# Performance work log

Measured on AMD Instinct MI355X. Metric: run time of the kernel, lower is better.

## Reference

```python
import jax, jax.numpy as jnp
import numpy as np

N_NODES = 100000
HIDDEN = 64
N_LAYERS = 4
N_EDGES = 800000
EPS = 1e-5  # equinox RMSNorm default


def rmsnorm(x, w):
    # per-node RMSNorm over last dim, learned scale, no bias
    inv = jax.lax.rsqrt(jnp.mean(x * x, axis=-1, keepdims=True) + EPS)
    return x * inv * w


def setup_inputs() -> dict:
    key = jax.random.key(0)
    ks = jax.random.split(key, 5)
    x = jax.random.normal(ks[0], (N_NODES, HIDDEN), dtype=jnp.float32)
    # eqx Linear weight (out,in), init ~ U(-1/sqrt(in), 1/sqrt(in)); randn*scale is fine for a baseline
    scale = 1.0 / np.sqrt(HIDDEN)
    conv_w = jax.random.normal(ks[1], (N_LAYERS, HIDDEN, HIDDEN), dtype=jnp.float32) * scale
    hid_w = jax.random.normal(ks[2], (N_LAYERS, HIDDEN, HIDDEN), dtype=jnp.float32) * scale
    conv_norm_w = jnp.ones((N_LAYERS, HIDDEN), dtype=jnp.float32)
    hid_norm_w = jnp.ones((N_LAYERS, HIDDEN), dtype=jnp.float32)
    row = jax.random.randint(ks[3], (N_EDGES,), 0, N_NODES, dtype=jnp.int32)
    col = jax.random.randint(ks[4], (N_EDGES,), 0, N_NODES, dtype=jnp.int32)
    return {"x": x, "conv_w": conv_w, "conv_norm_w": conv_norm_w,
            "hid_w": hid_w, "hid_norm_w": hid_norm_w, "row": row, "col": col}


def reference(x, conv_w, conv_norm_w, hid_w, hid_norm_w, row, col):
    n_nodes = x.shape[0]

    def step(h, params):
        cw, cnw, hw, hnw = params
        # GConvLayer: linear (no bias) -> relu -> sparse adjacency aggregation -> residual RMSNorm
        m = jax.nn.relu(h @ cw.T)                                  # [n_nodes, d]
        agg = jax.ops.segment_sum(m[col], row, num_segments=n_nodes)  # a @ m (unweighted COO)
        h = rmsnorm(h + agg, cnw)
        # HiddenLayer: linear -> relu -> residual RMSNorm
        y = jax.nn.relu(h @ hw.T)
        h = rmsnorm(h + y, hnw)
        return h, None

    x, _ = jax.lax.scan(step, x, (conv_w, conv_norm_w, hid_w, hid_norm_w))
    return x
```

## Files before the change

### kernel.cpp

```cpp
#include <hip/hip_runtime.h>
#include <hip/hip_bf16.h>

#define HIDDEN 64
#define EPS 1e-5f
#define NPB 64
#define NPB2 128
#define WST 72

typedef __attribute__((ext_vector_type(8))) short bf16x8;
typedef __attribute__((ext_vector_type(4))) float f32x4;

__device__ __forceinline__ unsigned short f2b(float x) {
    __hip_bfloat16 b = __float2bfloat16(x);
    return *(unsigned short*)&b;
}
__device__ __forceinline__ float b2f(unsigned short u) {
    unsigned int ui = (unsigned int)u << 16;
    return *(float*)&ui;
}
__device__ __forceinline__ float b2f_lo(unsigned int u) { unsigned int ui = u << 16; return *(float*)&ui; }
__device__ __forceinline__ float b2f_hi(unsigned int u) { unsigned int ui = u & 0xffff0000u; return *(float*)&ui; }


__global__ __launch_bounds__(256) void hist_rank_kernel(const int* __restrict__ row,
                                                        int* __restrict__ cnt,
                                                        int* __restrict__ erank, int e) {
    int stride = gridDim.x * blockDim.x;
    for (int i = blockIdx.x * blockDim.x + threadIdx.x; i < e; i += stride) {
        int r = row[i];
        erank[i] = atomicAdd(&cnt[r], 1);
    }
}

__global__ __launch_bounds__(256) void block_sum_kernel(const int* __restrict__ cnt,
                                                        int* __restrict__ bsum, int n) {
    __shared__ int wsum[4];
    int tid = threadIdx.x;
    int i = blockIdx.x * 256 + tid;
    int v = (i < n) ? cnt[i] : 0;
#pragma unroll
    for (int off = 32; off > 0; off >>= 1) v += __shfl_xor(v, off, 64);
    if ((tid & 63) == 0) wsum[tid >> 6] = v;
    __syncthreads();
    if (tid == 0) bsum[blockIdx.x] = wsum[0] + wsum[1] + wsum[2] + wsum[3];
}

__global__ __launch_bounds__(1024) void scan_bsum_kernel(int* __restrict__ bsum, int nb,
                                                         int* __restrict__ total_out) {
    __shared__ int wsum[16];
    __shared__ int wexcl[16];
    int tid = threadIdx.x;
    int lane = tid & 63;
    int w = tid >> 6;
    int v = (tid < nb) ? bsum[tid] : 0;
    int sc = v;
#pragma unroll
    for (int off = 1; off < 64; off <<= 1) {
        int t = __shfl_up(sc, off, 64);
        if (lane >= off) sc += t;
    }
    if (lane == 63) wsum[w] = sc;
    __syncthreads();
    if (tid == 0) {
        int a = 0;
#pragma unroll
        for (int j = 0; j < 16; j++) { wexcl[j] = a; a += wsum[j]; }
        *total_out = a;
    }
    __syncthreads();
    if (tid < nb) bsum[tid] = wexcl[w] + (sc - v);
}

__global__ __launch_bounds__(256) void scan_final_kernel(const int* __restrict__ cnt,
                                                         const int* __restrict__ bexcl,
                                                         int* __restrict__ row_ptr, int n) {
    __shared__ int wsum[4];
    __shared__ int wexcl[4];
    int tid = threadIdx.x;
    int lane = tid & 63;
    int w = tid >> 6;
    int i = blockIdx.x * 256 + tid;
    int v = (i < n) ? cnt[i] : 0;
    int sc = v;
#pragma unroll
    for (int off = 1; off < 64; off <<= 1) {
        int t = __shfl_up(sc, off, 64);
        if (lane >= off) sc += t;
    }
    if (lane == 63) wsum[w] = sc;
    __syncthreads();
    if (tid == 0) {
        int a = 0;
#pragma unroll
        for (int j = 0; j < 4; j++) { wexcl[j] = a; a += wsum[j]; }
    }
    __syncthreads();
    if (i < n) row_ptr[i] = bexcl[blockIdx.x] + wexcl[w] + (sc - v);
}

__global__ __launch_bounds__(256) void fill_kernel(const int* __restrict__ row,
                                                   const int* __restrict__ col,
                                                   const int* __restrict__ row_ptr,
                                                   const int* __restrict__ erank,
                                                   int* __restrict__ ecol, int e, int n) {
    int cls = blockIdx.x & 7;
    int sub = blockIdx.x >> 3;
    int nsub = gridDim.x >> 3;
    int lo = (int)(((long long)n * cls) >> 3);
    int hi = (int)(((long long)n * (cls + 1)) >> 3);
    for (int i = sub * 256 + threadIdx.x; i < e; i += nsub * 256) {
        int r = row[i];
        if (r >= lo && r < hi) {
            int pos = row_ptr[r] + erank[i];
            ecol[pos] = col[i];
        }
    }
}

__global__ __launch_bounds__(256) void wconv_kernel(const float* __restrict__ cw,
                                                    const float* __restrict__ hw,
                                                    unsigned short* __restrict__ wbt, int L) {
    int idx = blockIdx.x * blockDim.x + threadIdx.x;
    int total = 2 * L * 4096;
    if (idx >= total) return;
    int mat = idx >> 12;
    int rem = idx & 4095;
    const float* src = (mat < L) ? (cw + (size_t)mat * 4096) : (hw + (size_t)(mat - L) * 4096);
    wbt[idx] = f2b(src[rem]);
}


__device__ __forceinline__ void mfma_tile(const unsigned short* s_a,
                                          const unsigned short* s_b,
                                          int l16, int quad, int wbase, f32x4 acc[4]) {
    const unsigned short* ap = &s_a[(size_t)(wbase + l16) * WST + quad * 8];
    const unsigned short* bp = &s_b[(size_t)l16 * WST + quad * 8];
#pragma unroll
    for (int kt = 0; kt < 2; kt++) {
        bf16x8 a = *(const bf16x8*)(ap + kt * 32);
#pragma unroll
        for (int nt = 0; nt < 4; nt++) {
            bf16x8 b = *(const bf16x8*)(bp + (size_t)nt * 16 * WST + kt * 32);
            acc[nt] = __builtin_amdgcn_mfma_f32_16x16x32_bf16(a, b, acc[nt], 0, 0, 0);
        }
    }
}

__device__ __forceinline__ void stage_wb(const unsigned short* __restrict__ wsrc,
                                         unsigned short* s_wb, int tid) {
    for (int i = tid; i < 512; i += 256) {
        int r = i >> 3, seg = i & 7;
        *(uint4*)(&s_wb[r * WST + seg * 8]) = ((const uint4*)(wsrc + r * 64))[seg];
    }
}


__global__ __launch_bounds__(256) void mm_relu_kernel(const float* __restrict__ h,
                                                      const unsigned short* __restrict__ wb,
                                                      __hip_bfloat16* __restrict__ m, int n) {
    __shared__ unsigned short s_hb[NPB * WST];
    __shared__ unsigned short s_wb[64 * WST];
    int tid = threadIdx.x;
    int base = blockIdx.x * NPB;
    stage_wb(wb, s_wb, tid);
    for (int i = tid; i < 512; i += 256) {
        int r = i >> 3, seg = i & 7;
        if (base + r < n) {
            const float4* hp = (const float4*)(h + (size_t)(base + r) * HIDDEN + seg * 8);
            float4 ha = hp[0], hb = hp[1];
            uint4 p;
            p.x = (unsigned int)f2b(ha.x) | ((unsigned int)f2b(ha.y) << 16);
            p.y = (unsigned int)f2b(ha.z) | ((unsigned int)f2b(ha.w) << 16);
            p.z = (unsigned int)f2b(hb.x) | ((unsigned int)f2b(hb.y) << 16);
            p.w = (unsigned int)f2b(hb.z) | ((unsigned int)f2b(hb.w) << 16);
            *(uint4*)(&s_hb[r * WST + seg * 8]) = p;
        } else {
            *(uint4*)(&s_hb[r * WST + seg * 8]) = make_uint4(0u, 0u, 0u, 0u);
        }
    }
    __syncthreads();
    int lane = tid & 63, wave = tid >> 6;
    int quad = lane >> 4, l16 = lane & 15;
    int wbase = wave * 16;
    f32x4 acc[4];
    acc[0] = (f32x4){0.f,0.f,0.f,0.f}; acc[1] = (f32x4){0.f,0.f,0.f,0.f};
    acc[2] = (f32x4){0.f,0.f,0.f,0.f}; acc[3] = (f32x4){0.f,0.f,0.f,0.f};
    mfma_tile(s_hb, s_wb, l16, quad, wbase, acc);
    unsigned short* mo = (unsigned short*)m;
#pragma unroll
    for (int r = 0; r < 4; r++) {
        int node = base + wbase + quad * 4 + r;
        if (node < n) {
#pragma unroll
            for (int nt = 0; nt < 4; nt++)
                mo[(size_t)node * HIDDEN + nt * 16 + l16] = f2b(fmaxf(acc[nt][r], 0.f));
        }
    }
}

__global__ __launch_bounds__(256) void aggregate_kernel(const float* hf,
                                                        const __hip_bfloat16* hb_in,
                                                        const __hip_bfloat16* __restrict__ m,
                                                        const int* __restrict__ row_ptr,
                                                        const int* __restrict__ ecol,
                                                        const float* __restrict__ nw,
                                                        __hip_bfloat16* __restrict__ hb_out,
                                                        int n) {
    int lane = threadIdx.x & 63;
    int wave = (blockIdx.x * blockDim.x + threadIdx.x) >> 6;
    int grp = lane >> 3;
    int sl = lane & 7;
    int node = 8 * wave + grp;
    if (node >= n) return;
    int beg = row_ptr[node];
    int end = row_ptr[node + 1];
    float s[8];
    if (hf) {
        const float4* hp = (const float4*)(hf + (size_t)node * HIDDEN + 8 * sl);
        float4 v0 = hp[0], v1 = hp[1];
        s[0] = v0.x; s[1] = v0.y; s[2] = v0.z; s[3] = v0.w;
        s[4] = v1.x; s[5] = v1.y; s[6] = v1.z; s[7] = v1.w;
    } else {
        uint4 u = *(const uint4*)((const unsigned short*)hb_in + (size_t)node * HIDDEN + 8 * sl);
        s[0] = b2f_lo(u.x); s[1] = b2f_hi(u.x);
        s[2] = b2f_lo(u.y); s[3] = b2f_hi(u.y);
        s[4] = b2f_lo(u.z); s[5] = b2f_hi(u.z);
        s[6] = b2f_lo(u.w); s[7] = b2f_hi(u.w);
    }
    const unsigned short* mi = (const unsigned short*)m;
    float p0[8], p1[8];
#pragma unroll
    for (int q = 0; q < 8; q++) { p0[q] = 0.f; p1[q] = 0.f; }
    int sbase = grp * 8;
    for (int b0 = beg; b0 < end; b0 += 8) {
        int idx = b0 + sl;
        int myc = ecol[idx < end ? idx : end - 1];
        int cnt = end - b0;
        if (cnt > 8) cnt = 8;
        int c[8];
#pragma unroll
        for (int j = 0; j < 8; j++) c[j] = __shfl(myc, sbase + j, 64);
        uint4 u[8];
#pragma unroll
        for (int j = 0; j < 8; j++)
            u[j] = *(const uint4*)(mi + (size_t)c[j] * HIDDEN + 8 * sl);
#pragma unroll
        for (int j = 0; j < 8; j++) {
            bool ok = j < cnt;
            float* p = (j & 1) ? p1 : p0;
            p[0] += ok ? b2f_lo(u[j].x) : 0.f;
            p[1] += ok ? b2f_hi(u[j].x) : 0.f;
            p[2] += ok ? b2f_lo(u[j].y) : 0.f;
            p[3] += ok ? b2f_hi(u[j].y) : 0.f;
            p[4] += ok ? b2f_lo(u[j].z) : 0.f;
            p[5] += ok ? b2f_hi(u[j].z) : 0.f;
            p[6] += ok ? b2f_lo(u[j].w) : 0.f;
            p[7] += ok ? b2f_hi(u[j].w) : 0.f;
        }
    }
    float ss = 0.f;
#pragma unroll
    for (int q = 0; q < 8; q++) {
        s[q] += p0[q] + p1[q];
        ss += s[q] * s[q];
    }
#pragma unroll
    for (int off = 4; off > 0; off >>= 1) ss += __shfl_xor(ss, off, 64);
    float inv = rsqrtf(ss * (1.0f / 64.0f) + EPS);
    const float4* nwp = (const float4*)(nw + 8 * sl);
    float4 w0 = nwp[0], w1 = nwp[1];
    uint4 pb;
    pb.x = (unsigned int)f2b(s[0] * inv * w0.x) | ((unsigned int)f2b(s[1] * inv * w0.y) << 16);
    pb.y = (unsigned int)f2b(s[2] * inv * w0.z) | ((unsigned int)f2b(s[3] * inv * w0.w) << 16);
    pb.z = (unsigned int)f2b(s[4] * inv * w1.x) | ((unsigned int)f2b(s[5] * inv * w1.y) << 16);
    pb.w = (unsigned int)f2b(s[6] * inv * w1.z) | ((unsigned int)f2b(s[7] * inv * w1.w) << 16);
    *(uint4*)((unsigned short*)hb_out + (size_t)node * HIDDEN + 8 * sl) = pb;
}


__global__ __launch_bounds__(256) void hidden_next_kernel(const __hip_bfloat16* __restrict__ hb_in,
                                                          const unsigned short* __restrict__ hwb,
                                                          const unsigned short* cwb_next,
                                                          const float* __restrict__ hnw,
                                                          float* out_f32,
                                                          __hip_bfloat16* hb_new,
                                                          __hip_bfloat16* m_out, int n) {
    __shared__ unsigned short s_hb[NPB2 * WST];
    __shared__ unsigned short s_wb[64 * WST];
    __shared__ unsigned short s_wb2[64 * WST];
    int tid = threadIdx.x;
    int base = blockIdx.x * NPB2;
    stage_wb(hwb, s_wb, tid);
    if (cwb_next) stage_wb(cwb_next, s_wb2, tid);
    const unsigned short* hbs = (const unsigned short*)hb_in;
    for (int i = tid; i < 1024; i += 256) {
        int r = i >> 3, seg = i & 7;
        uint4 p = make_uint4(0u, 0u, 0u, 0u);
        if (base + r < n) p = ((const uint4*)(hbs + (size_t)(base + r) * HIDDEN))[seg];
        *(uint4*)(&s_hb[r * WST + seg * 8]) = p;
    }
    __syncthreads();

    int lane = tid & 63, wave = tid >> 6;
    int quad = lane >> 4, l16 = lane & 15;

    float nwv[4];
#pragma unroll
    for (int nt = 0; nt < 4; nt++) nwv[nt] = hnw[nt * 16 + l16];

#pragma unroll
    for (int t = 0; t < 2; t++) {
        int wbase = wave * 16 + t * 64;

        f32x4 acc[4];
        acc[0] = (f32x4){0.f,0.f,0.f,0.f}; acc[1] = (f32x4){0.f,0.f,0.f,0.f};
        acc[2] = (f32x4){0.f,0.f,0.f,0.f}; acc[3] = (f32x4){0.f,0.f,0.f,0.f};
        mfma_tile(s_hb, s_wb, l16, quad, wbase, acc);

        float hv[4][4];
        float ssq[4] = {0.f, 0.f, 0.f, 0.f};
#pragma unroll
        for (int r = 0; r < 4; r++) {
            int nl = wbase + quad * 4 + r;
#pragma unroll
            for (int nt = 0; nt < 4; nt++) {
                float hres = b2f(s_hb[(size_t)nl * WST + nt * 16 + l16]);
                float v = hres + fmaxf(acc[nt][r], 0.f);
                hv[r][nt] = v;
                ssq[r] += v * v;
            }
        }
#pragma unroll
        for (int mk = 1; mk <= 8; mk <<= 1) {
#pragma unroll
            for (int r = 0; r < 4; r++) ssq[r] += __shfl_xor(ssq[r], mk, 64);
        }
#pragma unroll
        for (int r = 0; r < 4; r++) {
            float inv = rsqrtf(ssq[r] * (1.0f / 64.0f) + EPS);
#pragma unroll
            for (int nt = 0; nt < 4; nt++) hv[r][nt] *= inv * nwv[nt];
        }
        if (out_f32) {
#pragma unroll
            for (int r = 0; r < 4; r++) {
                int node = base + wbase + quad * 4 + r;
                if (node < n) {
#pragma unroll
                    for (int nt = 0; nt < 4; nt++)
                        out_f32[(size_t)node * HIDDEN + nt * 16 + l16] = hv[r][nt];
                }
            }
        }
        if (hb_new) {
            unsigned short* ho = (unsigned short*)hb_new;
#pragma unroll
            for (int r = 0; r < 4; r++) {
                int node = base + wbase + quad * 4 + r;
                if (node < n) {
#pragma unroll
                    for (int nt = 0; nt < 4; nt++)
                        ho[(size_t)node * HIDDEN + nt * 16 + l16] = f2b(hv[r][nt]);
                }
            }
        }

        if (!m_out) continue;

#pragma unroll
        for (int r = 0; r < 4; r++) {
            int nl = wbase + quad * 4 + r;
#pragma unroll
            for (int nt = 0; nt < 4; nt++)
                s_hb[(size_t)nl * WST + nt * 16 + l16] = f2b(hv[r][nt]);
        }

        f32x4 acc2[4];
        acc2[0] = (f32x4){0.f,0.f,0.f,0.f}; acc2[1] = (f32x4){0.f,0.f,0.f,0.f};
        acc2[2] = (f32x4){0.f,0.f,0.f,0.f}; acc2[3] = (f32x4){0.f,0.f,0.f,0.f};
        mfma_tile(s_hb, s_wb2, l16, quad, wbase, acc2);
        unsigned short* mo = (unsigned short*)m_out;
#pragma unroll
        for (int r = 0; r < 4; r++) {
            int node = base + wbase + quad * 4 + r;
            if (node < n) {
#pragma unroll
                for (int nt = 0; nt < 4; nt++)
                    mo[(size_t)node * HIDDEN + nt * 16 + l16] = f2b(fmaxf(acc2[nt][r], 0.f));
            }
        }
    }
}


static inline size_t align_up(size_t x, size_t a) { return (x + a - 1) & ~(a - 1); }

extern "C" void kernel_launch(void* const* d_in, const int* in_sizes, int n_in,
                              void* d_out, int out_size, void* d_ws, size_t ws_size,
                              hipStream_t stream) {
    const float* x       = (const float*)d_in[0];
    const float* conv_w  = (const float*)d_in[1];
    const float* conv_nw = (const float*)d_in[2];
    const float* hid_w   = (const float*)d_in[3];
    const float* hid_nw  = (const float*)d_in[4];
    const int*   row     = (const int*)d_in[5];
    const int*   col     = (const int*)d_in[6];
    float* out = (float*)d_out;

    const int n = in_sizes[0] / HIDDEN;
    const int e = in_sizes[5];
    const int L = in_sizes[1] / 4096;

    size_t off = 0;
    char* ws = (char*)d_ws;
    __hip_bfloat16* mA = (__hip_bfloat16*)(ws + off);  off = align_up(off + (size_t)n * HIDDEN * 2, 16);
    __hip_bfloat16* mB = (__hip_bfloat16*)(ws + off);  off = align_up(off + (size_t)n * HIDDEN * 2, 16);
    __hip_bfloat16* hb1 = (__hip_bfloat16*)(ws + off); off = align_up(off + (size_t)n * HIDDEN * 2, 16);
    __hip_bfloat16* hb2 = (__hip_bfloat16*)(ws + off); off = align_up(off + (size_t)n * HIDDEN * 2, 16);
    unsigned short* wbt = (unsigned short*)(ws + off); off = align_up(off + (size_t)2 * L * 4096 * 2, 16);
    int* row_ptr = (int*)(ws + off);           off = align_up(off + (size_t)(n + 1) * 4, 16);
    int* cnt = (int*)(ws + off);               off = align_up(off + (size_t)n * 4, 16);
    int* bsum = (int*)(ws + off);              off = align_up(off + (size_t)1024 * 4, 16);
    int* erank = (int*)(ws + off);             off = align_up(off + (size_t)e * 4, 16);
    int* ecol = (int*)(ws + off);              off = align_up(off + (size_t)e * 4, 16);

    const int nb = (n + 255) / 256;

    hipMemsetAsync(cnt, 0, (size_t)n * 4, stream);
    hist_rank_kernel<<<1024, 256, 0, stream>>>(row, cnt, erank, e);
    block_sum_kernel<<<nb, 256, 0, stream>>>(cnt, bsum, n);
    scan_bsum_kernel<<<1, 1024, 0, stream>>>(bsum, nb, row_ptr + n);
    scan_final_kernel<<<nb, 256, 0, stream>>>(cnt, bsum, row_ptr, n);
    fill_kernel<<<1024, 256, 0, stream>>>(row, col, row_ptr, erank, ecol, e, n);

    wconv_kernel<<<(2 * L * 4096 + 255) / 256, 256, 0, stream>>>(conv_w, hid_w, wbt, L);

    const int blocks = (n + NPB - 1) / NPB;
    const int hblocks = (n + NPB2 - 1) / NPB2;
    const int agg_blocks = (((n + 7) / 8) * 64 + 255) / 256;

    mm_relu_kernel<<<blocks, 256, 0, stream>>>(x, wbt, mA, n);

    const __hip_bfloat16* mi = mA;
    __hip_bfloat16* mo = mB;
    for (int l = 0; l < L; l++) {
        aggregate_kernel<<<agg_blocks, 256, 0, stream>>>(
            (l == 0) ? x : nullptr, (l == 0) ? nullptr : hb2, mi, row_ptr, ecol,
            conv_nw + (size_t)l * HIDDEN, hb1, n);
        bool last = (l == L - 1);
        hidden_next_kernel<<<hblocks, 256, 0, stream>>>(
            hb1, wbt + (size_t)(L + l) * 4096,
            last ? nullptr : (wbt + (size_t)(l + 1) * 4096),
            hid_nw + (size_t)l * HIDDEN,
            last ? out : nullptr,
            last ? nullptr : hb2,
            last ? nullptr : mo, n);
        __hip_bfloat16* tmp = (__hip_bfloat16*)mi; mi = mo; mo = tmp;
    }
}
```

Measured before the change: 285.8 us.

## Fuse aggregation into hidden-layer kernel and merge scan kernels

Aggregation and RMSNorm now happen inside the same kernel as the hidden linear and next conv linear, so the normalized conv output is placed in shared memory instead of written to and reread from global memory. This removes one launch and one bf16 round trip per layer, and ping-pongs the hidden-state buffers so reads and writes never alias. The separate block-sum scan kernel is also dropped: each scan block sums its preceding block totals itself, which is redundant work that grows with block index but saves a launch. The fused kernel uses 64-node blocks, and its irregular gather latency now sits in the same block as the MFMA work, which may lower occupancy or reduce overlap.

```diff
diff --git a/kernel.cpp b/kernel.cpp
--- a/kernel.cpp
+++ b/kernel.cpp
@@ -4,7 +4,6 @@
 #define HIDDEN 64
 #define EPS 1e-5f
 #define NPB 64
-#define NPB2 128
 #define WST 72
 
 typedef __attribute__((ext_vector_type(8))) short bf16x8;
@@ -45,14 +44,26 @@
     if (tid == 0) bsum[blockIdx.x] = wsum[0] + wsum[1] + wsum[2] + wsum[3];
 }
 
-__global__ __launch_bounds__(1024) void scan_bsum_kernel(int* __restrict__ bsum, int nb,
-                                                         int* __restrict__ total_out) {
-    __shared__ int wsum[16];
-    __shared__ int wexcl[16];
+__global__ __launch_bounds__(256) void scan_final_kernel(const int* __restrict__ cnt,
+                                                         const int* __restrict__ bsum,
+                                                         int* __restrict__ row_ptr,
+                                                         int n, int nb) {
+    __shared__ int wred[4];
+    __shared__ int wsum[4];
+    __shared__ int wexcl[4];
+    __shared__ int s_prev;
+    __shared__ int s_tot;
+    int b = blockIdx.x;
     int tid = threadIdx.x;
     int lane = tid & 63;
     int w = tid >> 6;
-    int v = (tid < nb) ? bsum[tid] : 0;
+    int acc = 0;
+    for (int j = tid; j < b; j += 256) acc += bsum[j];
+#pragma unroll
+    for (int off = 32; off > 0; off >>= 1) acc += __shfl_xor(acc, off, 64);
+    if (lane == 0) wred[w] = acc;
+    int i = b * 256 + tid;
+    int v = (i < n) ? cnt[i] : 0;
     int sc = v;
 #pragma unroll
     for (int off = 1; off < 64; off <<= 1) {
@@ -62,40 +73,15 @@
     if (lane == 63) wsum[w] = sc;
     __syncthreads();
     if (tid == 0) {
+        s_prev = wred[0] + wred[1] + wred[2] + wred[3];
         int a = 0;
 #pragma unroll
-        for (int j = 0; j < 16; j++) { wexcl[j] = a; a += wsum[j]; }
-        *total_out = a;
+        for (int j = 0; j < 4; j++) { wexcl[j] = a; a += wsum[j]; }
+        s_tot = a;
     }
     __syncthreads();
-    if (tid < nb) bsum[tid] = wexcl[w] + (sc - v);
-}
-
-__global__ __launch_bounds__(256) void scan_final_kernel(const int* __restrict__ cnt,
-                                                         const int* __restrict__ bexcl,
-                                                         int* __restrict__ row_ptr, int n) {
-    __shared__ int wsum[4];
-    __shared__ int wexcl[4];
-    int tid = threadIdx.x;
-    int lane = tid & 63;
-    int w = tid >> 6;
-    int i = blockIdx.x * 256 + tid;
-    int v = (i < n) ? cnt[i] : 0;
-    int sc = v;
-#pragma unroll
-    for (int off = 1; off < 64; off <<= 1) {
-        int t = __shfl_up(sc, off, 64);
-        if (lane >= off) sc += t;
-    }
-    if (lane == 63) wsum[w] = sc;
-    __syncthreads();
-    if (tid == 0) {
-        int a = 0;
-#pragma unroll
-        for (int j = 0; j < 4; j++) { wexcl[j] = a; a += wsum[j]; }
-    }
-    __syncthreads();
-    if (i < n) row_ptr[i] = bexcl[blockIdx.x] + wexcl[w] + (sc - v);
+    if (i < n) row_ptr[i] = s_prev + wexcl[w] + (sc - v);
+    if (b == nb - 1 && tid == 0) row_ptr[n] = s_prev + s_tot;
 }
 
 __global__ __launch_bounds__(256) void fill_kernel(const int* __restrict__ row,
@@ -198,196 +184,180 @@
     }
 }
 
-__global__ __launch_bounds__(256) void aggregate_kernel(const float* hf,
-                                                        const __hip_bfloat16* hb_in,
-                                                        const __hip_bfloat16* __restrict__ m,
-                                                        const int* __restrict__ row_ptr,
-                                                        const int* __restrict__ ecol,
-                                                        const float* __restrict__ nw,
-                                                        __hip_bfloat16* __restrict__ hb_out,
-                                                        int n) {
-    int lane = threadIdx.x & 63;
-    int wave = (blockIdx.x * blockDim.x + threadIdx.x) >> 6;
-    int grp = lane >> 3;
-    int sl = lane & 7;
-    int node = 8 * wave + grp;
-    if (node >= n) return;
-    int beg = row_ptr[node];
-    int end = row_ptr[node + 1];
-    float s[8];
-    if (hf) {
-        const float4* hp = (const float4*)(hf + (size_t)node * HIDDEN + 8 * sl);
-        float4 v0 = hp[0], v1 = hp[1];
-        s[0] = v0.x; s[1] = v0.y; s[2] = v0.z; s[3] = v0.w;
-        s[4] = v1.x; s[5] = v1.y; s[6] = v1.z; s[7] = v1.w;
-    } else {
-        uint4 u = *(const uint4*)((const unsigned short*)hb_in + (size_t)node * HIDDEN + 8 * sl);
-        s[0] = b2f_lo(u.x); s[1] = b2f_hi(u.x);
-        s[2] = b2f_lo(u.y); s[3] = b2f_hi(u.y);
-        s[4] = b2f_lo(u.z); s[5] = b2f_hi(u.z);
-        s[6] = b2f_lo(u.w); s[7] = b2f_hi(u.w);
-    }
-    const unsigned short* mi = (const unsigned short*)m;
-    float p0[8], p1[8];
-#pragma unroll
-    for (int q = 0; q < 8; q++) { p0[q] = 0.f; p1[q] = 0.f; }
-    int sbase = grp * 8;
-    for (int b0 = beg; b0 < end; b0 += 8) {
-        int idx = b0 + sl;
-        int myc = ecol[idx < end ? idx : end - 1];
-        int cnt = end - b0;
-        if (cnt > 8) cnt = 8;
-        int c[8];
-#pragma unroll
-        for (int j = 0; j < 8; j++) c[j] = __shfl(myc, sbase + j, 64);
-        uint4 u[8];
-#pragma unroll
-        for (int j = 0; j < 8; j++)
-            u[j] = *(const uint4*)(mi + (size_t)c[j] * HIDDEN + 8 * sl);
-#pragma unroll
-        for (int j = 0; j < 8; j++) {
-            bool ok = j < cnt;
-            float* p = (j & 1) ? p1 : p0;
-            p[0] += ok ? b2f_lo(u[j].x) : 0.f;
-            p[1] += ok ? b2f_hi(u[j].x) : 0.f;
-            p[2] += ok ? b2f_lo(u[j].y) : 0.f;
-            p[3] += ok ? b2f_hi(u[j].y) : 0.f;
-            p[4] += ok ? b2f_lo(u[j].z) : 0.f;
-            p[5] += ok ? b2f_hi(u[j].z) : 0.f;
-            p[6] += ok ? b2f_lo(u[j].w) : 0.f;
-            p[7] += ok ? b2f_hi(u[j].w) : 0.f;
-        }
-    }
-    float ss = 0.f;
-#pragma unroll
-    for (int q = 0; q < 8; q++) {
-        s[q] += p0[q] + p1[q];
-        ss += s[q] * s[q];
-    }
-#pragma unroll
-    for (int off = 4; off > 0; off >>= 1) ss += __shfl_xor(ss, off, 64);
-    float inv = rsqrtf(ss * (1.0f / 64.0f) + EPS);
-    const float4* nwp = (const float4*)(nw + 8 * sl);
-    float4 w0 = nwp[0], w1 = nwp[1];
-    uint4 pb;
-    pb.x = (unsigned int)f2b(s[0] * inv * w0.x) | ((unsigned int)f2b(s[1] * inv * w0.y) << 16);
-    pb.y = (unsigned int)f2b(s[2] * inv * w0.z) | ((unsigned int)f2b(s[3] * inv * w0.w) << 16);
-    pb.z = (unsigned int)f2b(s[4] * inv * w1.x) | ((unsigned int)f2b(s[5] * inv * w1.y) << 16);
-    pb.w = (unsigned int)f2b(s[6] * inv * w1.z) | ((unsigned int)f2b(s[7] * inv * w1.w) << 16);
-    *(uint4*)((unsigned short*)hb_out + (size_t)node * HIDDEN + 8 * sl) = pb;
-}
-
-
-__global__ __launch_bounds__(256) void hidden_next_kernel(const __hip_bfloat16* __restrict__ hb_in,
-                                                          const unsigned short* __restrict__ hwb,
-                                                          const unsigned short* cwb_next,
-                                                          const float* __restrict__ hnw,
-                                                          float* out_f32,
-                                                          __hip_bfloat16* hb_new,
-                                                          __hip_bfloat16* m_out, int n) {
-    __shared__ unsigned short s_hb[NPB2 * WST];
+
+__global__ __launch_bounds__(256) void fused_layer_kernel(
+        const float* hf, const __hip_bfloat16* hb_in,
+        const __hip_bfloat16* __restrict__ m_in,
+        const unsigned short* __restrict__ hwb,
+        const unsigned short* cwb_next,
+        const int* __restrict__ row_ptr, const int* __restrict__ ecol,
+        const float* __restrict__ cnw, const float* __restrict__ hnw,
+        float* out_f32, __hip_bfloat16* hb_new, __hip_bfloat16* m_out, int n) {
+    __shared__ unsigned short s_hb[NPB * WST];
     __shared__ unsigned short s_wb[64 * WST];
     __shared__ unsigned short s_wb2[64 * WST];
     int tid = threadIdx.x;
-    int base = blockIdx.x * NPB2;
+    int base = blockIdx.x * NPB;
+    int lane = tid & 63, wave = tid >> 6;
+
     stage_wb(hwb, s_wb, tid);
     if (cwb_next) stage_wb(cwb_next, s_wb2, tid);
-    const unsigned short* hbs = (const unsigned short*)hb_in;
-    for (int i = tid; i < 1024; i += 256) {
-        int r = i >> 3, seg = i & 7;
-        uint4 p = make_uint4(0u, 0u, 0u, 0u);
-        if (base + r < n) p = ((const uint4*)(hbs + (size_t)(base + r) * HIDDEN))[seg];
-        *(uint4*)(&s_hb[r * WST + seg * 8]) = p;
-    }
-    __syncthreads();
-
-    int lane = tid & 63, wave = tid >> 6;
-    int quad = lane >> 4, l16 = lane & 15;
-
-    float nwv[4];
-#pragma unroll
-    for (int nt = 0; nt < 4; nt++) nwv[nt] = hnw[nt * 16 + l16];
-
-#pragma unroll
-    for (int t = 0; t < 2; t++) {
-        int wbase = wave * 16 + t * 64;
-
-        f32x4 acc[4];
-        acc[0] = (f32x4){0.f,0.f,0.f,0.f}; acc[1] = (f32x4){0.f,0.f,0.f,0.f};
-        acc[2] = (f32x4){0.f,0.f,0.f,0.f}; acc[3] = (f32x4){0.f,0.f,0.f,0.f};
-        mfma_tile(s_hb, s_wb, l16, quad, wbase, acc);
-
-        float hv[4][4];
-        float ssq[4] = {0.f, 0.f, 0.f, 0.f};
-#pragma unroll
-        for (int r = 0; r < 4; r++) {
-            int nl = wbase + quad * 4 + r;
-#pragma unroll
-            for (int nt = 0; nt < 4; nt++) {
-                float hres = b2f(s_hb[(size_t)nl * WST + nt * 16 + l16]);
-                float v = hres + fmaxf(acc[nt][r], 0.f);
-                hv[r][nt] = v;
-                ssq[r] += v * v;
+
+    int grp = lane >> 3;
+    int sl = lane & 7;
+    int sbase = grp * 8;
+    const float4* cp = (const float4*)(cnw + 8 * sl);
+    float4 c0 = cp[0], c1 = cp[1];
+    const unsigned short* mi = (const unsigned short*)m_in;
+
+#pragma unroll
+    for (int rnd = 0; rnd < 2; rnd++) {
+        int nl = wave * 16 + rnd * 8 + grp;
+        int node = base + nl;
+        uint4 pb = make_uint4(0u, 0u, 0u, 0u);
+        if (node < n) {
+            float s[8];
+            if (hf) {
+                const float4* hp = (const float4*)(hf + (size_t)node * HIDDEN + 8 * sl);
+                float4 v0 = hp[0], v1 = hp[1];
+                s[0] = v0.x; s[1] = v0.y; s[2] = v0.z; s[3] = v0.w;
+                s[4] = v1.x; s[5] = v1.y; s[6] = v1.z; s[7] = v1.w;
+            } else {
+                uint4 u = *(const uint4*)((const unsigned short*)hb_in + (size_t)node * HIDDEN + 8 * sl);
+                s[0] = b2f_lo(u.x); s[1] = b2f_hi(u.x);
+                s[2] = b2f_lo(u.y); s[3] = b2f_hi(u.y);
+                s[4] = b2f_lo(u.z); s[5] = b2f_hi(u.z);
+                s[6] = b2f_lo(u.w); s[7] = b2f_hi(u.w);
             }
-        }
-#pragma unroll
-        for (int mk = 1; mk <= 8; mk <<= 1) {
-#pragma unroll
-            for (int r = 0; r < 4; r++) ssq[r] += __shfl_xor(ssq[r], mk, 64);
-        }
-#pragma unroll
-        for (int r = 0; r < 4; r++) {
-            float inv = rsqrtf(ssq[r] * (1.0f / 64.0f) + EPS);
-#pragma unroll
-            for (int nt = 0; nt < 4; nt++) hv[r][nt] *= inv * nwv[nt];
-        }
-        if (out_f32) {
-#pragma unroll
-            for (int r = 0; r < 4; r++) {
-                int node = base + wbase + quad * 4 + r;
-                if (node < n) {
-#pragma unroll
-                    for (int nt = 0; nt < 4; nt++)
-                        out_f32[(size_t)node * HIDDEN + nt * 16 + l16] = hv[r][nt];
+            int beg = row_ptr[node];
+            int end = row_ptr[node + 1];
+            float p0[8], p1[8];
+#pragma unroll
+            for (int q = 0; q < 8; q++) { p0[q] = 0.f; p1[q] = 0.f; }
+            for (int b0 = beg; b0 < end; b0 += 8) {
+                int idx = b0 + sl;
+                int myc = ecol[idx < end ? idx : end - 1];
+                int cnt = end - b0;
+                if (cnt > 8) cnt = 8;
+                int c[8];
+#pragma unroll
+                for (int j = 0; j < 8; j++) c[j] = __shfl(myc, sbase + j, 64);
+                uint4 u[8];
+#pragma unroll
+                for (int j = 0; j < 8; j++)
+                    u[j] = *(const uint4*)(mi + (size_t)c[j] * HIDDEN + 8 * sl);
+#pragma unroll
+                for (int j = 0; j < 8; j++) {
+                    bool ok = j < cnt;
+                    float* p = (j & 1) ? p1 : p0;
+                    p[0] += ok ? b2f_lo(u[j].x) : 0.f;
+                    p[1] += ok ? b2f_hi(u[j].x) : 0.f;
+                    p[2] += ok ? b2f_lo(u[j].y) : 0.f;
+                    p[3] += ok ? b2f_hi(u[j].y) : 0.f;
+                    p[4] += ok ? b2f_lo(u[j].z) : 0.f;
+                    p[5] += ok ? b2f_hi(u[j].z) : 0.f;
+                    p[6] += ok ? b2f_lo(u[j].w) : 0.f;
+                    p[7] += ok ? b2f_hi(u[j].w) : 0.f;
                 }
             }
-        }
-        if (hb_new) {
-            unsigned short* ho = (unsigned short*)hb_new;
-#pragma unroll
-            for (int r = 0; r < 4; r++) {
-                int node = base + wbase + quad * 4 + r;
-                if (node < n) {
-#pragma unroll
-                    for (int nt = 0; nt < 4; nt++)
-                        ho[(size_t)node * HIDDEN + nt * 16 + l16] = f2b(hv[r][nt]);
-                }
+            float ss = 0.f;
+#pragma unroll
+            for (int q = 0; q < 8; q++) {
+                s[q] += p0[q] + p1[q];
+                ss += s[q] * s[q];
             }
-        }
-
-        if (!m_out) continue;
-
-#pragma unroll
-        for (int r = 0; r < 4; r++) {
-            int nl = wbase + quad * 4 + r;
-#pragma unroll
-            for (int nt = 0; nt < 4; nt++)
-                s_hb[(size_t)nl * WST + nt * 16 + l16] = f2b(hv[r][nt]);
-        }
-
-        f32x4 acc2[4];
-        acc2[0] = (f32x4){0.f,0.f,0.f,0.f}; acc2[1] = (f32x4){0.f,0.f,0.f,0.f};
-        acc2[2] = (f32x4){0.f,0.f,0.f,0.f}; acc2[3] = (f32x4){0.f,0.f,0.f,0.f};
-        mfma_tile(s_hb, s_wb2, l16, quad, wbase, acc2);
-        unsigned short* mo = (unsigned short*)m_out;
+#pragma unroll
+            for (int off = 4; off > 0; off >>= 1) ss += __shfl_xor(ss, off, 64);
+            float inv = rsqrtf(ss * (1.0f / 64.0f) + EPS);
+            pb.x = (unsigned int)f2b(s[0] * inv * c0.x) | ((unsigned int)f2b(s[1] * inv * c0.y) << 16);
+            pb.y = (unsigned int)f2b(s[2] * inv * c0.z) | ((unsigned int)f2b(s[3] * inv * c0.w) << 16);
+            pb.z = (unsigned int)f2b(s[4] * inv * c1.x) | ((unsigned int)f2b(s[5] * inv * c1.y) << 16);
+            pb.w = (unsigned int)f2b(s[6] * inv * c1.z) | ((unsigned int)f2b(s[7] * inv * c1.w) << 16);
+        }
+        *(uint4*)(&s_hb[(size_t)nl * WST + 8 * sl]) = pb;
+    }
+    __syncthreads();
+
+    int quad = lane >> 4, l16 = lane & 15;
+    int wbase = wave * 16;
+    f32x4 acc[4];
+    acc[0] = (f32x4){0.f,0.f,0.f,0.f}; acc[1] = (f32x4){0.f,0.f,0.f,0.f};
+    acc[2] = (f32x4){0.f,0.f,0.f,0.f}; acc[3] = (f32x4){0.f,0.f,0.f,0.f};
+    mfma_tile(s_hb, s_wb, l16, quad, wbase, acc);
+
+    float hv[4][4];
+    float ssq[4] = {0.f, 0.f, 0.f, 0.f};
+#pragma unroll
+    for (int r = 0; r < 4; r++) {
+        int nl = wbase + quad * 4 + r;
+#pragma unroll
+        for (int nt = 0; nt < 4; nt++) {
+            float hres = b2f(s_hb[(size_t)nl * WST + nt * 16 + l16]);
+            float v = hres + fmaxf(acc[nt][r], 0.f);
+            hv[r][nt] = v;
+            ssq[r] += v * v;
+        }
+    }
+#pragma unroll
+    for (int mk = 1; mk <= 8; mk <<= 1) {
+#pragma unroll
+        for (int r = 0; r < 4; r++) ssq[r] += __shfl_xor(ssq[r], mk, 64);
+    }
+    float nwv[4];
+#pragma unroll
+    for (int nt = 0; nt < 4; nt++) nwv[nt] = hnw[nt * 16 + l16];
+#pragma unroll
+    for (int r = 0; r < 4; r++) {
+        float inv = rsqrtf(ssq[r] * (1.0f / 64.0f) + EPS);
+#pragma unroll
+        for (int nt = 0; nt < 4; nt++) hv[r][nt] *= inv * nwv[nt];
+    }
+    if (out_f32) {
 #pragma unroll
         for (int r = 0; r < 4; r++) {
             int node = base + wbase + quad * 4 + r;
             if (node < n) {
 #pragma unroll
                 for (int nt = 0; nt < 4; nt++)
-                    mo[(size_t)node * HIDDEN + nt * 16 + l16] = f2b(fmaxf(acc2[nt][r], 0.f));
+                    out_f32[(size_t)node * HIDDEN + nt * 16 + l16] = hv[r][nt];
             }
+        }
+    }
+    if (hb_new) {
+        unsigned short* ho = (unsigned short*)hb_new;
+#pragma unroll
+        for (int r = 0; r < 4; r++) {
+            int node = base + wbase + quad * 4 + r;
+            if (node < n) {
+#pragma unroll
+                for (int nt = 0; nt < 4; nt++)
+                    ho[(size_t)node * HIDDEN + nt * 16 + l16] = f2b(hv[r][nt]);
+            }
+        }
+    }
+
+    if (!m_out) return;
+
+#pragma unroll
+    for (int r = 0; r < 4; r++) {
+        int nl = wbase + quad * 4 + r;
+#pragma unroll
+        for (int nt = 0; nt < 4; nt++)
+            s_hb[(size_t)nl * WST + nt * 16 + l16] = f2b(hv[r][nt]);
+    }
+
+    f32x4 acc2[4];
+    acc2[0] = (f32x4){0.f,0.f,0.f,0.f}; acc2[1] = (f32x4){0.f,0.f,0.f,0.f};
+    acc2[2] = (f32x4){0.f,0.f,0.f,0.f}; acc2[3] = (f32x4){0.f,0.f,0.f,0.f};
+    mfma_tile(s_hb, s_wb2, l16, quad, wbase, acc2);
+    unsigned short* mo = (unsigned short*)m_out;
+#pragma unroll
+    for (int r = 0; r < 4; r++) {
+        int node = base + wbase + quad * 4 + r;
+        if (node < n) {
+#pragma unroll
+            for (int nt = 0; nt < 4; nt++)
+                mo[(size_t)node * HIDDEN + nt * 16 + l16] = f2b(fmaxf(acc2[nt][r], 0.f));
         }
     }
 }
@@ -429,32 +399,32 @@
     hipMemsetAsync(cnt, 0, (size_t)n * 4, stream);
     hist_rank_kernel<<<1024, 256, 0, stream>>>(row, cnt, erank, e);
     block_sum_kernel<<<nb, 256, 0, stream>>>(cnt, bsum, n);
-    scan_bsum_kernel<<<1, 1024, 0, stream>>>(bsum, nb, row_ptr + n);
-    scan_final_kernel<<<nb, 256, 0, stream>>>(cnt, bsum, row_ptr, n);
+    scan_final_kernel<<<nb, 256, 0, stream>>>(cnt, bsum, row_ptr, n, nb);
     fill_kernel<<<1024, 256, 0, stream>>>(row, col, row_ptr, erank, ecol, e, n);
 
     wconv_kernel<<<(2 * L * 4096 + 255) / 256, 256, 0, stream>>>(conv_w, hid_w, wbt, L);
 
     const int blocks = (n + NPB - 1) / NPB;
-    const int hblocks = (n + NPB2 - 1) / NPB2;
-    const int agg_blocks = (((n + 7) / 8) * 64 + 255) / 256;
 
     mm_relu_kernel<<<blocks, 256, 0, stream>>>(x, wbt, mA, n);
 
     const __hip_bfloat16* mi = mA;
     __hip_bfloat16* mo = mB;
+    __hip_bfloat16* hin = nullptr;
+    __hip_bfloat16* hout = hb1;
     for (int l = 0; l < L; l++) {
-        aggregate_kernel<<<agg_blocks, 256, 0, stream>>>(
-            (l == 0) ? x : nullptr, (l == 0) ? nullptr : hb2, mi, row_ptr, ecol,
-            conv_nw + (size_t)l * HIDDEN, hb1, n);
         bool last = (l == L - 1);
-        hidden_next_kernel<<<hblocks, 256, 0, stream>>>(
-            hb1, wbt + (size_t)(L + l) * 4096,
+        fused_layer_kernel<<<blocks, 256, 0, stream>>>(
+            (l == 0) ? x : nullptr, hin, mi,
+            wbt + (size_t)(L + l) * 4096,
             last ? nullptr : (wbt + (size_t)(l + 1) * 4096),
-            hid_nw + (size_t)l * HIDDEN,
+            row_ptr, ecol,
+            conv_nw + (size_t)l * HIDDEN, hid_nw + (size_t)l * HIDDEN,
             last ? out : nullptr,
-            last ? nullptr : hb2,
+            last ? nullptr : hout,
             last ? nullptr : mo, n);
         __hip_bfloat16* tmp = (__hip_bfloat16*)mi; mi = mo; mo = tmp;
-    }
-}
+        hin = hout;
+        hout = (hout == hb1) ? hb2 : hb1;
+    }
+}
```

After: 274.5 us. -3.9%, faster.
